# Optimization experiments

Hardware: AMD Instinct MI355X
Metric: run time of the kernel (lower is better)

The kernel has to match this reference:

```python
import jax, jax.numpy as jnp
import numpy as np

N_NODES = 100000
N_EDGES = 800000
N_GRAPHS = 256
IN_C = 96
HID = 96
OUT_C = 16


def setup_inputs() -> dict:
    key = jax.random.key(0)
    ks = jax.random.split(key, 10)
    x = jax.random.normal(ks[0], (N_NODES, IN_C), dtype=jnp.float32)
    edge_index = jax.random.randint(ks[1], (2, N_EDGES), 0, N_NODES, dtype=jnp.int64)
    batch = jnp.sort(jax.random.randint(ks[2], (N_NODES,), 0, N_GRAPHS, dtype=jnp.int64))
    def glorot(k, fan_in, fan_out):
        s = np.sqrt(6.0 / (fan_in + fan_out)).astype(np.float32)
        return jax.random.uniform(k, (fan_in, fan_out), minval=-s, maxval=s, dtype=jnp.float32)
    W1 = glorot(ks[3], IN_C, HID)
    W2 = glorot(ks[4], HID, HID)
    W3 = glorot(ks[5], HID, HID)
    Wlin = glorot(ks[6], HID, OUT_C)
    b1 = jnp.zeros((HID,), dtype=jnp.float32)
    b2 = jnp.zeros((HID,), dtype=jnp.float32)
    b3 = jnp.zeros((HID,), dtype=jnp.float32)
    return {"x": x, "edge_index": edge_index, "batch": batch,
            "W1": W1, "b1": b1, "W2": W2, "b2": b2, "W3": W3, "b3": b3, "Wlin": Wlin}


def _gcn_conv(x, W, b, src, dst):
    # PyG GCNConv(normalize=True): add self-loops, deg includes self-loop,
    # norm_ij = deg_i^{-1/2} * deg_j^{-1/2}; linear (no bias) then scatter-add; bias after.
    n = x.shape[0]
    deg = jnp.zeros((n,), dtype=x.dtype).at[dst].add(1.0) + 1.0  # +1 self-loop
    dinv = jax.lax.rsqrt(deg)
    h = x @ W                                   # [N, H]
    coef = dinv[src] * dinv[dst]                # [E]
    msg = h[src] * coef[:, None]                # [E, H] gather
    agg = jax.ops.segment_sum(msg, dst, num_segments=n)  # scatter-add
    agg = agg + h * (dinv * dinv)[:, None]      # self-loop contribution
    return agg + b


def reference(x, edge_index, batch, W1, b1, W2, b2, W3, b3, Wlin):
    src, dst = edge_index[0], edge_index[1]
    h = jax.nn.relu(_gcn_conv(x, W1, b1, src, dst))
    h = jax.nn.relu(_gcn_conv(h, W2, b2, src, dst))
    h = _gcn_conv(h, W3, b3, src, dst)
    # global mean pool over graphs
    sums = jax.ops.segment_sum(h, batch, num_segments=N_GRAPHS)
    counts = jax.ops.segment_sum(jnp.ones((h.shape[0],), dtype=h.dtype), batch, num_segments=N_GRAPHS)
    pooled = sums / jnp.maximum(counts, 1.0)[:, None]
    return pooled @ Wlin
```

## Files before the change

### kernel.cpp

```cpp
#include <hip/hip_runtime.h>

#define NN 100000
#define NE 800000
#define NG 256
#define CH 96
#define OC 16
#define NBLK 391
#define TM 128
#define GBLK 782

typedef __attribute__((ext_vector_type(8))) short bf16x8;
typedef __attribute__((ext_vector_type(4))) float f32x4;

__device__ __forceinline__ unsigned short f2bf(float x) {
    unsigned u = __float_as_uint(x);
    return (unsigned short)((u + 0x7fffu + ((u >> 16) & 1u)) >> 16);
}
__device__ __forceinline__ float bf2f(unsigned short h) {
    return __uint_as_float(((unsigned)h) << 16);
}
__device__ __forceinline__ void split8(const float4 a, const float4 b,
                                       bf16x8& hi, bf16x8& lo) {
    float v[8] = {a.x, a.y, a.z, a.w, b.x, b.y, b.z, b.w};
#pragma unroll
    for (int j = 0; j < 8; j++) {
        unsigned short h = f2bf(v[j]);
        hi[j] = (short)h;
        lo[j] = (short)f2bf(v[j] - bf2f(h));
    }
}
__device__ __forceinline__ float4 us4_to_f4(ushort4 u) {
    return make_float4(bf2f(u.x), bf2f(u.y), bf2f(u.z), bf2f(u.w));
}
__device__ __forceinline__ void unpack8(uint4 v, float* f) {
    f[0] = __uint_as_float(v.x << 16); f[1] = __uint_as_float(v.x & 0xffff0000u);
    f[2] = __uint_as_float(v.y << 16); f[3] = __uint_as_float(v.y & 0xffff0000u);
    f[4] = __uint_as_float(v.z << 16); f[5] = __uint_as_float(v.z & 0xffff0000u);
    f[6] = __uint_as_float(v.w << 16); f[7] = __uint_as_float(v.w & 0xffff0000u);
}

__global__ __launch_bounds__(256) void k_init(int* __restrict__ cntp,
                                              int* __restrict__ gtot,
                                              const float* __restrict__ W1,
                                              const float* __restrict__ W2,
                                              const float* __restrict__ W3,
                                              unsigned short* __restrict__ WH,
                                              unsigned short* __restrict__ WL) {
    int id = blockIdx.x * 256 + threadIdx.x;
    if (id < NN) {
        uint4 z = {0u, 0u, 0u, 0u};
        uint4* p = reinterpret_cast<uint4*>(&cntp[(size_t)id * 16]);
        p[0] = z; p[1] = z; p[2] = z; p[3] = z;
    }
    if (id == 0) *gtot = 0;
    if (id < 3 * CH * CH) {
        int w = id / (CH * CH);
        int r = id - w * (CH * CH);
        int k = r / CH;
        int n = r - k * CH;
        const float* Ws = (w == 0) ? W1 : (w == 1) ? W2 : W3;
        float v = Ws[k * CH + n];
        unsigned short h = f2bf(v);
        WH[w * CH * CH + n * CH + k] = h;
        WL[w * CH * CH + n * CH + k] = f2bf(v - bf2f(h));
    }
}

__global__ __launch_bounds__(256) void k_front(const float* __restrict__ X,
                                               const unsigned short* __restrict__ WH,
                                               const unsigned short* __restrict__ WL,
                                               unsigned short* __restrict__ H,
                                               const int* __restrict__ dst,
                                               int* __restrict__ cntp,
                                               int* __restrict__ slot) {
    __shared__ __align__(16) unsigned short WsH[CH * CH];
    __shared__ __align__(16) unsigned short WsL[CH * CH];

    const int tid = threadIdx.x;

    if (blockIdx.x >= GBLK) {
        int e = (blockIdx.x - GBLK) * 256 + tid;
        slot[e] = atomicAdd(&cntp[(size_t)dst[e] * 16], 1);
        return;
    }

    const int n0 = blockIdx.x * TM;
    {
        const uint4* sH = reinterpret_cast<const uint4*>(WH);
        const uint4* sL = reinterpret_cast<const uint4*>(WL);
        uint4* dH = reinterpret_cast<uint4*>(WsH);
        uint4* dL = reinterpret_cast<uint4*>(WsL);
        for (int i = tid; i < CH * CH / 8; i += 256) {
            dH[i] = sH[i];
            dL[i] = sL[i];
        }
    }
    __syncthreads();

    const int lane = tid & 63;
    const int wave = tid >> 6;
    const int lrow = lane & 15;
    const int quad = lane >> 4;

    const float4* X4 = reinterpret_cast<const float4*>(X);

    f32x4 acc[2][6];
#pragma unroll
    for (int rt = 0; rt < 2; rt++)
#pragma unroll
        for (int ct = 0; ct < 6; ct++) acc[rt][ct] = (f32x4){0.f, 0.f, 0.f, 0.f};

    int arow[2];
#pragma unroll
    for (int rt = 0; rt < 2; rt++)
        arow[rt] = min(n0 + (wave * 2 + rt) * 16 + lrow, NN - 1);

#pragma unroll
    for (int kc = 0; kc < 3; kc++) {
        bf16x8 ahi[2], alo[2];
#pragma unroll
        for (int rt = 0; rt < 2; rt++) {
            int fo = (arow[rt] * CH + kc * 32 + quad * 8) >> 2;
            split8(X4[fo], X4[fo + 1], ahi[rt], alo[rt]);
        }
#pragma unroll
        for (int ct = 0; ct < 6; ct++) {
            int bo = (ct * 16 + lrow) * CH + kc * 32 + quad * 8;
            bf16x8 bhi = *reinterpret_cast<const bf16x8*>(&WsH[bo]);
            bf16x8 blo = *reinterpret_cast<const bf16x8*>(&WsL[bo]);
#pragma unroll
            for (int rt = 0; rt < 2; rt++) {
                acc[rt][ct] = __builtin_amdgcn_mfma_f32_16x16x32_bf16(
                    alo[rt], bhi, acc[rt][ct], 0, 0, 0);
                acc[rt][ct] = __builtin_amdgcn_mfma_f32_16x16x32_bf16(
                    ahi[rt], blo, acc[rt][ct], 0, 0, 0);
                acc[rt][ct] = __builtin_amdgcn_mfma_f32_16x16x32_bf16(
                    ahi[rt], bhi, acc[rt][ct], 0, 0, 0);
            }
        }
    }

#pragma unroll
    for (int rt = 0; rt < 2; rt++) {
        int rbase = n0 + (wave * 2 + rt) * 16 + quad * 4;
#pragma unroll
        for (int ct = 0; ct < 6; ct++) {
            int col = ct * 16 + lrow;
#pragma unroll
            for (int r = 0; r < 4; r++) {
                int row = rbase + r;
                if (row < NN) H[(size_t)row * CH + col] = f2bf(acc[rt][ct][r]);
            }
        }
    }
}

__global__ __launch_bounds__(256) void k_offsets(const int* __restrict__ cntp,
                                                 int* __restrict__ cntc,
                                                 int* __restrict__ gtot,
                                                 int* __restrict__ off,
                                                 float* __restrict__ dinv,
                                                 const int* __restrict__ batch,
                                                 int* __restrict__ goff) {
    int i = blockIdx.x * 256 + threadIdx.x;
    int lane = threadIdx.x & 63;
    int c = (i < NN) ? cntp[(size_t)i * 16] : 0;

    int incl = c;
#pragma unroll
    for (int d = 1; d < 64; d <<= 1) {
        int t = __shfl_up(incl, d);
        if (lane >= d) incl += t;
    }
    int total = __shfl(incl, 63);
    int base = 0;
    if (lane == 63) base = atomicAdd(gtot, total);
    base = __shfl(base, 63);

    if (i >= NN) return;
    cntc[i] = c;
    off[i] = base + incl - c;
    dinv[i] = rsqrtf((float)c + 1.0f);
    int b = batch[i];
    int bp = (i > 0) ? batch[i - 1] : -1;
    for (int g = bp + 1; g <= b; g++) goff[g] = i;
    if (i == NN - 1)
        for (int g = b + 1; g <= NG; g++) goff[g] = NN;
}

__global__ __launch_bounds__(256) void k_build(const int* __restrict__ src,
                                               const int* __restrict__ dst,
                                               const int* __restrict__ off,
                                               const int* __restrict__ slot,
                                               const float* __restrict__ dinv,
                                               float2* __restrict__ packed) {
    int e = blockIdx.x * 256 + threadIdx.x;
    int s = src[e];
    int d = dst[e];
    packed[off[d] + slot[e]] = make_float2(__int_as_float(s), dinv[s] * dinv[d]);
}

__global__ __launch_bounds__(256) void k_gemm_bf16(const unsigned short* __restrict__ X,
                                                   const unsigned short* __restrict__ WH,
                                                   const unsigned short* __restrict__ WL,
                                                   unsigned short* __restrict__ H) {
    __shared__ __align__(16) unsigned short WsH[CH * CH];
    __shared__ __align__(16) unsigned short WsL[CH * CH];

    const int tid = threadIdx.x;
    const int n0 = blockIdx.x * TM;

    {
        const uint4* sH = reinterpret_cast<const uint4*>(WH);
        const uint4* sL = reinterpret_cast<const uint4*>(WL);
        uint4* dH = reinterpret_cast<uint4*>(WsH);
        uint4* dL = reinterpret_cast<uint4*>(WsL);
        for (int i = tid; i < CH * CH / 8; i += 256) {
            dH[i] = sH[i];
            dL[i] = sL[i];
        }
    }
    __syncthreads();

    const int lane = tid & 63;
    const int wave = tid >> 6;
    const int lrow = lane & 15;
    const int quad = lane >> 4;

    f32x4 acc[2][6];
#pragma unroll
    for (int rt = 0; rt < 2; rt++)
#pragma unroll
        for (int ct = 0; ct < 6; ct++) acc[rt][ct] = (f32x4){0.f, 0.f, 0.f, 0.f};

    int arow[2];
#pragma unroll
    for (int rt = 0; rt < 2; rt++)
        arow[rt] = min(n0 + (wave * 2 + rt) * 16 + lrow, NN - 1);

#pragma unroll
    for (int kc = 0; kc < 3; kc++) {
        bf16x8 ahi[2];
#pragma unroll
        for (int rt = 0; rt < 2; rt++)
            ahi[rt] = *reinterpret_cast<const bf16x8*>(
                &X[(size_t)arow[rt] * CH + kc * 32 + quad * 8]);
#pragma unroll
        for (int ct = 0; ct < 6; ct++) {
            int bo = (ct * 16 + lrow) * CH + kc * 32 + quad * 8;
            bf16x8 bhi = *reinterpret_cast<const bf16x8*>(&WsH[bo]);
            bf16x8 blo = *reinterpret_cast<const bf16x8*>(&WsL[bo]);
#pragma unroll
            for (int rt = 0; rt < 2; rt++) {
                acc[rt][ct] = __builtin_amdgcn_mfma_f32_16x16x32_bf16(
                    ahi[rt], blo, acc[rt][ct], 0, 0, 0);
                acc[rt][ct] = __builtin_amdgcn_mfma_f32_16x16x32_bf16(
                    ahi[rt], bhi, acc[rt][ct], 0, 0, 0);
            }
        }
    }

#pragma unroll
    for (int rt = 0; rt < 2; rt++) {
        int rbase = n0 + (wave * 2 + rt) * 16 + quad * 4;
#pragma unroll
        for (int ct = 0; ct < 6; ct++) {
            int col = ct * 16 + lrow;
#pragma unroll
            for (int r = 0; r < 4; r++) {
                int row = rbase + r;
                if (row < NN) H[(size_t)row * CH + col] = f2bf(acc[rt][ct][r]);
            }
        }
    }
}

template <bool RELU>
__global__ __launch_bounds__(256) void k_aggregate(const int* __restrict__ off,
                                                   const int* __restrict__ cnt,
                                                   const float2* __restrict__ packed,
                                                   const float* __restrict__ dinv,
                                                   const float* __restrict__ bias,
                                                   const unsigned short* __restrict__ H,
                                                   unsigned short* __restrict__ Bout) {
    int idx = blockIdx.x * 256 + threadIdx.x;
    if (idx >= NN * 12) return;
    int n = idx / 12;
    int c8 = idx - n * 12;
    int e0 = off[n];
    int e1 = e0 + cnt[n];

    const uint4* H8 = reinterpret_cast<const uint4*>(H);

    float a[8];
    {
        float hf[8];
        unpack8(H8[(size_t)n * 12 + c8], hf);
        float di = dinv[n];
        float d2 = di * di;
        const float4* bias4 = reinterpret_cast<const float4*>(bias);
        float4 b0 = bias4[c8 * 2], b1 = bias4[c8 * 2 + 1];
        float bf[8] = {b0.x, b0.y, b0.z, b0.w, b1.x, b1.y, b1.z, b1.w};
#pragma unroll
        for (int j = 0; j < 8; j++) a[j] = hf[j] * d2 + bf[j];
    }

    int e = e0;
    for (; e + 4 <= e1; e += 4) {
        float2 p0 = packed[e + 0];
        float2 p1 = packed[e + 1];
        float2 p2 = packed[e + 2];
        float2 p3 = packed[e + 3];
        uint4 v0 = H8[(size_t)__float_as_int(p0.x) * 12 + c8];
        uint4 v1 = H8[(size_t)__float_as_int(p1.x) * 12 + c8];
        uint4 v2 = H8[(size_t)__float_as_int(p2.x) * 12 + c8];
        uint4 v3 = H8[(size_t)__float_as_int(p3.x) * 12 + c8];
        float f0[8], f1[8], f2[8], f3[8];
        unpack8(v0, f0); unpack8(v1, f1); unpack8(v2, f2); unpack8(v3, f3);
#pragma unroll
        for (int j = 0; j < 8; j++)
            a[j] += f0[j] * p0.y + f1[j] * p1.y + f2[j] * p2.y + f3[j] * p3.y;
    }
    for (; e < e1; e++) {
        float2 pc = packed[e];
        uint4 v = H8[(size_t)__float_as_int(pc.x) * 12 + c8];
        float f[8];
        unpack8(v, f);
#pragma unroll
        for (int j = 0; j < 8; j++) a[j] += f[j] * pc.y;
    }
    if (RELU) {
#pragma unroll
        for (int j = 0; j < 8; j++) a[j] = fmaxf(a[j], 0.0f);
    }
    uint4 o;
    o.x = (unsigned)f2bf(a[0]) | ((unsigned)f2bf(a[1]) << 16);
    o.y = (unsigned)f2bf(a[2]) | ((unsigned)f2bf(a[3]) << 16);
    o.z = (unsigned)f2bf(a[4]) | ((unsigned)f2bf(a[5]) << 16);
    o.w = (unsigned)f2bf(a[6]) | ((unsigned)f2bf(a[7]) << 16);
    reinterpret_cast<uint4*>(Bout)[(size_t)n * 12 + c8] = o;
}

__global__ __launch_bounds__(384) void k_pool_linear(const int* __restrict__ goff,
                                                     const unsigned short* __restrict__ B,
                                                     const float* __restrict__ Wlin,
                                                     float* __restrict__ out) {
    __shared__ float4 sh[16][24];
    __shared__ float pooled[CH];
    int g = blockIdx.x;
    int t = threadIdx.x;
    int nl = t / 24;
    int c4 = t - nl * 24;
    int s = goff[g];
    int e = goff[g + 1];

    float4 acc = make_float4(0.f, 0.f, 0.f, 0.f);
    const ushort4* B4 = reinterpret_cast<const ushort4*>(B);
    for (int n = s + nl; n < e; n += 16) {
        float4 v = us4_to_f4(B4[(size_t)n * 24 + c4]);
        acc.x += v.x; acc.y += v.y; acc.z += v.z; acc.w += v.w;
    }
    sh[nl][c4] = acc;
    __syncthreads();

    if (t < 24) {
        float4 r = make_float4(0.f, 0.f, 0.f, 0.f);
#pragma unroll
        for (int j = 0; j < 16; j++) {
            float4 v = sh[j][t];
            r.x += v.x; r.y += v.y; r.z += v.z; r.w += v.w;
        }
        float inv = 1.0f / fmaxf((float)(e - s), 1.0f);
        pooled[t * 4 + 0] = r.x * inv;
        pooled[t * 4 + 1] = r.y * inv;
        pooled[t * 4 + 2] = r.z * inv;
        pooled[t * 4 + 3] = r.w * inv;
    }
    __syncthreads();

    if (t < OC) {
        float a = 0.0f;
#pragma unroll 8
        for (int k = 0; k < CH; k++) a += pooled[k] * Wlin[k * OC + t];
        out[g * OC + t] = a;
    }
}

extern "C" void kernel_launch(void* const* d_in, const int* in_sizes, int n_in,
                              void* d_out, int out_size, void* d_ws, size_t ws_size,
                              hipStream_t stream) {
    const float* x = (const float*)d_in[0];
    const int* ei = (const int*)d_in[1];
    const int* src = ei;
    const int* dst = ei + NE;
    const int* batch = (const int*)d_in[2];
    const float* W1 = (const float*)d_in[3];
    const float* b1 = (const float*)d_in[4];
    const float* W2 = (const float*)d_in[5];
    const float* b2 = (const float*)d_in[6];
    const float* W3 = (const float*)d_in[7];
    const float* b3 = (const float*)d_in[8];
    const float* Wlin = (const float*)d_in[9];
    float* out = (float*)d_out;

    char* ws = (char*)d_ws;
    unsigned short* Ha = (unsigned short*)ws;  ws += (size_t)NN * CH * 2;
    unsigned short* Hb = (unsigned short*)ws;  ws += (size_t)NN * CH * 2;
    unsigned short* Bb = (unsigned short*)ws;  ws += (size_t)NN * CH * 2;
    float2* packed = (float2*)ws;   ws += (size_t)NE * 8;
    unsigned short* WH = (unsigned short*)ws;  ws += 3 * CH * CH * 2;
    unsigned short* WL = (unsigned short*)ws;  ws += 3 * CH * CH * 2;
    float* dinv = (float*)ws;       ws += NN * 4;
    int* off = (int*)ws;            ws += NN * 4;
    int* goff = (int*)ws;           ws += 272 * 4;
    int* cntc = (int*)ws;           ws += (NN + 4) * 4;
    int* gtot = cntc + NN;
    int* cntp = (int*)Hb;
    int* slot = (int*)Bb;

    k_init<<<NBLK, 256, 0, stream>>>(cntp, gtot, W1, W2, W3, WH, WL);
    k_front<<<GBLK + NE / 256, 256, 0, stream>>>(x, WH, WL, Ha, dst, cntp, slot);
    k_offsets<<<NBLK, 256, 0, stream>>>(cntp, cntc, gtot, off, dinv, batch, goff);
    k_build<<<NE / 256, 256, 0, stream>>>(src, dst, off, slot, dinv, packed);

    const int ablk = (NN * 12 + 255) / 256;

    k_aggregate<true><<<ablk, 256, 0, stream>>>(off, cntc, packed, dinv, b1, Ha, Bb);
    k_gemm_bf16<<<GBLK, 256, 0, stream>>>(Bb, WH + CH * CH, WL + CH * CH, Hb);
    k_aggregate<true><<<ablk, 256, 0, stream>>>(off, cntc, packed, dinv, b2, Hb, Bb);
    k_gemm_bf16<<<GBLK, 256, 0, stream>>>(Bb, WH + 2 * CH * CH, WL + 2 * CH * CH, Ha);
    k_aggregate<false><<<ablk, 256, 0, stream>>>(off, cntc, packed, dinv, b3, Ha, Bb);

    k_pool_linear<<<NG, 384, 0, stream>>>(goff, Bb, Wlin, out);
}
```

Before: 299.2 us.

## Split degree histogram into per-lane sub-counters and separate from first GEMM

The per-node degree counter changes from one 64-byte-padded int to four sub-counters picked by edge index mod 4, which spreads atomic contention on a node. k_offsets sums the four counters and writes a sub-offset for each, and k_build uses those to place edges. The histogram also moves out of the fused front kernel into its own launch before the layer-1 GEMM. This removes the fusion that let atomics overlap the GEMM, adds a kernel launch, and changes the order of edges within each node's neighbour list.

```diff
diff --git a/kernel.cpp b/kernel.cpp
--- a/kernel.cpp
+++ b/kernel.cpp
@@ -8,6 +8,7 @@
 #define NBLK 391
 #define TM 128
 #define GBLK 782
+#define HBLK 3125
 
 typedef __attribute__((ext_vector_type(8))) short bf16x8;
 typedef __attribute__((ext_vector_type(4))) float f32x4;
@@ -39,7 +40,7 @@
     f[6] = __uint_as_float(v.w << 16); f[7] = __uint_as_float(v.w & 0xffff0000u);
 }
 
-__global__ __launch_bounds__(256) void k_init(int* __restrict__ cntp,
+__global__ __launch_bounds__(256) void k_init(int* __restrict__ cnt4,
                                               int* __restrict__ gtot,
                                               const float* __restrict__ W1,
                                               const float* __restrict__ W2,
@@ -49,8 +50,7 @@
     int id = blockIdx.x * 256 + threadIdx.x;
     if (id < NN) {
         uint4 z = {0u, 0u, 0u, 0u};
-        uint4* p = reinterpret_cast<uint4*>(&cntp[(size_t)id * 16]);
-        p[0] = z; p[1] = z; p[2] = z; p[3] = z;
+        *reinterpret_cast<uint4*>(&cnt4[(size_t)id * 4]) = z;
     }
     if (id == 0) *gtot = 0;
     if (id < 3 * CH * CH) {
@@ -66,24 +66,21 @@
     }
 }
 
-__global__ __launch_bounds__(256) void k_front(const float* __restrict__ X,
+__global__ __launch_bounds__(256) void k_hist(const int* __restrict__ dst,
+                                              int* __restrict__ cnt4,
+                                              int* __restrict__ slot) {
+    int e = blockIdx.x * 256 + threadIdx.x;
+    slot[e] = atomicAdd(&cnt4[(size_t)dst[e] * 4 + (e & 3)], 1);
+}
+
+__global__ __launch_bounds__(256) void k_gemm1(const float* __restrict__ X,
                                                const unsigned short* __restrict__ WH,
                                                const unsigned short* __restrict__ WL,
-                                               unsigned short* __restrict__ H,
-                                               const int* __restrict__ dst,
-                                               int* __restrict__ cntp,
-                                               int* __restrict__ slot) {
+                                               unsigned short* __restrict__ H) {
     __shared__ __align__(16) unsigned short WsH[CH * CH];
     __shared__ __align__(16) unsigned short WsL[CH * CH];
 
     const int tid = threadIdx.x;
-
-    if (blockIdx.x >= GBLK) {
-        int e = (blockIdx.x - GBLK) * 256 + tid;
-        slot[e] = atomicAdd(&cntp[(size_t)dst[e] * 16], 1);
-        return;
-    }
-
     const int n0 = blockIdx.x * TM;
     {
         const uint4* sH = reinterpret_cast<const uint4*>(WH);
@@ -155,7 +152,7 @@
     }
 }
 
-__global__ __launch_bounds__(256) void k_offsets(const int* __restrict__ cntp,
+__global__ __launch_bounds__(256) void k_offsets(int* __restrict__ cnt4,
                                                  int* __restrict__ cntc,
                                                  int* __restrict__ gtot,
                                                  int* __restrict__ off,
@@ -164,7 +161,9 @@
                                                  int* __restrict__ goff) {
     int i = blockIdx.x * 256 + threadIdx.x;
     int lane = threadIdx.x & 63;
-    int c = (i < NN) ? cntp[(size_t)i * 16] : 0;
+    int4 c4 = {0, 0, 0, 0};
+    if (i < NN) c4 = *reinterpret_cast<const int4*>(&cnt4[(size_t)i * 4]);
+    int c = c4.x + c4.y + c4.z + c4.w;
 
     int incl = c;
 #pragma unroll
@@ -178,8 +177,15 @@
     base = __shfl(base, 63);
 
     if (i >= NN) return;
+    int myoff = base + incl - c;
     cntc[i] = c;
-    off[i] = base + incl - c;
+    off[i] = myoff;
+    int4 w;
+    w.x = myoff;
+    w.y = myoff + c4.x;
+    w.z = myoff + c4.x + c4.y;
+    w.w = myoff + c4.x + c4.y + c4.z;
+    *reinterpret_cast<int4*>(&cnt4[(size_t)i * 4]) = w;
     dinv[i] = rsqrtf((float)c + 1.0f);
     int b = batch[i];
     int bp = (i > 0) ? batch[i - 1] : -1;
@@ -190,14 +196,15 @@
 
 __global__ __launch_bounds__(256) void k_build(const int* __restrict__ src,
                                                const int* __restrict__ dst,
-                                               const int* __restrict__ off,
+                                               const int* __restrict__ cnt4,
                                                const int* __restrict__ slot,
                                                const float* __restrict__ dinv,
                                                float2* __restrict__ packed) {
     int e = blockIdx.x * 256 + threadIdx.x;
     int s = src[e];
     int d = dst[e];
-    packed[off[d] + slot[e]] = make_float2(__int_as_float(s), dinv[s] * dinv[d]);
+    int p = cnt4[(size_t)d * 4 + (e & 3)] + slot[e];
+    packed[p] = make_float2(__int_as_float(s), dinv[s] * dinv[d]);
 }
 
 __global__ __launch_bounds__(256) void k_gemm_bf16(const unsigned short* __restrict__ X,
@@ -415,13 +422,14 @@
     int* goff = (int*)ws;           ws += 272 * 4;
     int* cntc = (int*)ws;           ws += (NN + 4) * 4;
     int* gtot = cntc + NN;
-    int* cntp = (int*)Hb;
+    int* cnt4 = (int*)Hb;
     int* slot = (int*)Bb;
 
-    k_init<<<NBLK, 256, 0, stream>>>(cntp, gtot, W1, W2, W3, WH, WL);
-    k_front<<<GBLK + NE / 256, 256, 0, stream>>>(x, WH, WL, Ha, dst, cntp, slot);
-    k_offsets<<<NBLK, 256, 0, stream>>>(cntp, cntc, gtot, off, dinv, batch, goff);
-    k_build<<<NE / 256, 256, 0, stream>>>(src, dst, off, slot, dinv, packed);
+    k_init<<<NBLK, 256, 0, stream>>>(cnt4, gtot, W1, W2, W3, WH, WL);
+    k_hist<<<HBLK, 256, 0, stream>>>(dst, cnt4, slot);
+    k_gemm1<<<GBLK, 256, 0, stream>>>(x, WH, WL, Ha);
+    k_offsets<<<NBLK, 256, 0, stream>>>(cnt4, cntc, gtot, off, dinv, batch, goff);
+    k_build<<<NE / 256, 256, 0, stream>>>(src, dst, cnt4, slot, dinv, packed);
 
     const int ablk = (NN * 12 + 255) / 256;
 
```

Result: slower. 313.4 us (+4.7%).

## Fold final linear into layer-3 weights to aggregate 16 channels instead of 96

Applied to the files above, without the earlier changes.

Because the last GCN layer, mean pooling and the output linear are all linear, W3·Wlin and b3·Wlin are precomputed in the init kernel. The third GEMM then produces only 16 columns, and the third aggregation gathers 16-wide rows instead of 96-wide ones. This cuts the gather traffic of the last aggregation and the pooling work by about six times. In exchange, the fused weight is rounded to bf16 hi/lo, which slightly changes numerical rounding.

```diff
diff --git a/kernel.cpp b/kernel.cpp
--- a/kernel.cpp
+++ b/kernel.cpp
@@ -29,9 +29,6 @@
         lo[j] = (short)f2bf(v[j] - bf2f(h));
     }
 }
-__device__ __forceinline__ float4 us4_to_f4(ushort4 u) {
-    return make_float4(bf2f(u.x), bf2f(u.y), bf2f(u.z), bf2f(u.w));
-}
 __device__ __forceinline__ void unpack8(uint4 v, float* f) {
     f[0] = __uint_as_float(v.x << 16); f[1] = __uint_as_float(v.x & 0xffff0000u);
     f[2] = __uint_as_float(v.y << 16); f[3] = __uint_as_float(v.y & 0xffff0000u);
@@ -44,8 +41,11 @@
                                               const float* __restrict__ W1,
                                               const float* __restrict__ W2,
                                               const float* __restrict__ W3,
+                                              const float* __restrict__ b3,
+                                              const float* __restrict__ Wlin,
                                               unsigned short* __restrict__ WH,
-                                              unsigned short* __restrict__ WL) {
+                                              unsigned short* __restrict__ WL,
+                                              float* __restrict__ b3p) {
     int id = blockIdx.x * 256 + threadIdx.x;
     if (id < NN) {
         uint4 z = {0u, 0u, 0u, 0u};
@@ -53,16 +53,32 @@
         p[0] = z; p[1] = z; p[2] = z; p[3] = z;
     }
     if (id == 0) *gtot = 0;
-    if (id < 3 * CH * CH) {
+    if (id < 2 * CH * CH) {
         int w = id / (CH * CH);
         int r = id - w * (CH * CH);
         int k = r / CH;
         int n = r - k * CH;
-        const float* Ws = (w == 0) ? W1 : (w == 1) ? W2 : W3;
+        const float* Ws = (w == 0) ? W1 : W2;
         float v = Ws[k * CH + n];
         unsigned short h = f2bf(v);
         WH[w * CH * CH + n * CH + k] = h;
         WL[w * CH * CH + n * CH + k] = f2bf(v - bf2f(h));
+    } else if (id < 2 * CH * CH + CH * OC) {
+        int r = id - 2 * CH * CH;
+        int k = r / OC;
+        int oc = r - k * OC;
+        float v = 0.0f;
+#pragma unroll 8
+        for (int m = 0; m < CH; m++) v += W3[k * CH + m] * Wlin[m * OC + oc];
+        unsigned short h = f2bf(v);
+        WH[2 * CH * CH + oc * CH + k] = h;
+        WL[2 * CH * CH + oc * CH + k] = f2bf(v - bf2f(h));
+    } else if (id < 2 * CH * CH + CH * OC + OC) {
+        int oc = id - 2 * CH * CH - CH * OC;
+        float v = 0.0f;
+#pragma unroll 8
+        for (int m = 0; m < CH; m++) v += b3[m] * Wlin[m * OC + oc];
+        b3p[oc] = v;
     }
 }
 
@@ -271,6 +287,70 @@
                 int row = rbase + r;
                 if (row < NN) H[(size_t)row * CH + col] = f2bf(acc[rt][ct][r]);
             }
+        }
+    }
+}
+
+__global__ __launch_bounds__(256) void k_gemm3(const unsigned short* __restrict__ X,
+                                               const unsigned short* __restrict__ WH,
+                                               const unsigned short* __restrict__ WL,
+                                               unsigned short* __restrict__ H3) {
+    __shared__ __align__(16) unsigned short WsH[OC * CH];
+    __shared__ __align__(16) unsigned short WsL[OC * CH];
+
+    const int tid = threadIdx.x;
+    const int n0 = blockIdx.x * TM;
+
+    {
+        const uint4* sH = reinterpret_cast<const uint4*>(WH);
+        const uint4* sL = reinterpret_cast<const uint4*>(WL);
+        uint4* dH = reinterpret_cast<uint4*>(WsH);
+        uint4* dL = reinterpret_cast<uint4*>(WsL);
+        for (int i = tid; i < OC * CH / 8; i += 256) {
+            dH[i] = sH[i];
+            dL[i] = sL[i];
+        }
+    }
+    __syncthreads();
+
+    const int lane = tid & 63;
+    const int wave = tid >> 6;
+    const int lrow = lane & 15;
+    const int quad = lane >> 4;
+
+    f32x4 acc[2];
+#pragma unroll
+    for (int rt = 0; rt < 2; rt++) acc[rt] = (f32x4){0.f, 0.f, 0.f, 0.f};
+
+    int arow[2];
+#pragma unroll
+    for (int rt = 0; rt < 2; rt++)
+        arow[rt] = min(n0 + (wave * 2 + rt) * 16 + lrow, NN - 1);
+
+#pragma unroll
+    for (int kc = 0; kc < 3; kc++) {
+        bf16x8 ahi[2];
+#pragma unroll
+        for (int rt = 0; rt < 2; rt++)
+            ahi[rt] = *reinterpret_cast<const bf16x8*>(
+                &X[(size_t)arow[rt] * CH + kc * 32 + quad * 8]);
+        int bo = lrow * CH + kc * 32 + quad * 8;
+        bf16x8 bhi = *reinterpret_cast<const bf16x8*>(&WsH[bo]);
+        bf16x8 blo = *reinterpret_cast<const bf16x8*>(&WsL[bo]);
+#pragma unroll
+        for (int rt = 0; rt < 2; rt++) {
+            acc[rt] = __builtin_amdgcn_mfma_f32_16x16x32_bf16(ahi[rt], blo, acc[rt], 0, 0, 0);
+            acc[rt] = __builtin_amdgcn_mfma_f32_16x16x32_bf16(ahi[rt], bhi, acc[rt], 0, 0, 0);
+        }
+    }
+
+#pragma unroll
+    for (int rt = 0; rt < 2; rt++) {
+        int rbase = n0 + (wave * 2 + rt) * 16 + quad * 4;
+#pragma unroll
+        for (int r = 0; r < 4; r++) {
+            int row = rbase + r;
+            if (row < NN) H3[(size_t)row * OC + lrow] = f2bf(acc[rt][r]);
         }
     }
 }
@@ -341,48 +421,83 @@
     reinterpret_cast<uint4*>(Bout)[(size_t)n * 12 + c8] = o;
 }
 
-__global__ __launch_bounds__(384) void k_pool_linear(const int* __restrict__ goff,
-                                                     const unsigned short* __restrict__ B,
-                                                     const float* __restrict__ Wlin,
-                                                     float* __restrict__ out) {
-    __shared__ float4 sh[16][24];
-    __shared__ float pooled[CH];
+__global__ __launch_bounds__(256) void k_agg16(const int* __restrict__ off,
+                                               const int* __restrict__ cnt,
+                                               const float2* __restrict__ packed,
+                                               const float* __restrict__ dinv,
+                                               const unsigned short* __restrict__ H3,
+                                               float* __restrict__ B3) {
+    int idx = blockIdx.x * 256 + threadIdx.x;
+    if (idx >= NN * 2) return;
+    int n = idx >> 1;
+    int c8 = idx & 1;
+    int e0 = off[n];
+    int e1 = e0 + cnt[n];
+
+    const uint4* H8 = reinterpret_cast<const uint4*>(H3);
+
+    float a[8];
+    {
+        float hf[8];
+        unpack8(H8[(size_t)n * 2 + c8], hf);
+        float di = dinv[n];
+        float d2 = di * di;
+#pragma unroll
+        for (int j = 0; j < 8; j++) a[j] = hf[j] * d2;
+    }
+
+    int e = e0;
+    for (; e + 4 <= e1; e += 4) {
+        float2 p0 = packed[e + 0];
+        float2 p1 = packed[e + 1];
+        float2 p2 = packed[e + 2];
+        float2 p3 = packed[e + 3];
+        uint4 v0 = H8[(size_t)__float_as_int(p0.x) * 2 + c8];
+        uint4 v1 = H8[(size_t)__float_as_int(p1.x) * 2 + c8];
+        uint4 v2 = H8[(size_t)__float_as_int(p2.x) * 2 + c8];
+        uint4 v3 = H8[(size_t)__float_as_int(p3.x) * 2 + c8];
+        float f0[8], f1[8], f2[8], f3[8];
+        unpack8(v0, f0); unpack8(v1, f1); unpack8(v2, f2); unpack8(v3, f3);
+#pragma unroll
+        for (int j = 0; j < 8; j++)
+            a[j] += f0[j] * p0.y + f1[j] * p1.y + f2[j] * p2.y + f3[j] * p3.y;
+    }
+    for (; e < e1; e++) {
+        float2 pc = packed[e];
+        uint4 v = H8[(size_t)__float_as_int(pc.x) * 2 + c8];
+        float f[8];
+        unpack8(v, f);
+#pragma unroll
+        for (int j = 0; j < 8; j++) a[j] += f[j] * pc.y;
+    }
+
+    float4* B4 = reinterpret_cast<float4*>(B3);
+    B4[(size_t)n * 4 + c8 * 2 + 0] = make_float4(a[0], a[1], a[2], a[3]);
+    B4[(size_t)n * 4 + c8 * 2 + 1] = make_float4(a[4], a[5], a[6], a[7]);
+}
+
+__global__ __launch_bounds__(256) void k_pool16(const int* __restrict__ goff,
+                                                const float* __restrict__ B3,
+                                                const float* __restrict__ b3p,
+                                                float* __restrict__ out) {
+    __shared__ float sh[16][16];
     int g = blockIdx.x;
     int t = threadIdx.x;
-    int nl = t / 24;
-    int c4 = t - nl * 24;
+    int ch = t & 15;
+    int nl = t >> 4;
     int s = goff[g];
     int e = goff[g + 1];
 
-    float4 acc = make_float4(0.f, 0.f, 0.f, 0.f);
-    const ushort4* B4 = reinterpret_cast<const ushort4*>(B);
-    for (int n = s + nl; n < e; n += 16) {
-        float4 v = us4_to_f4(B4[(size_t)n * 24 + c4]);
-        acc.x += v.x; acc.y += v.y; acc.z += v.z; acc.w += v.w;
-    }
-    sh[nl][c4] = acc;
+    float acc = 0.0f;
+    for (int n = s + nl; n < e; n += 16) acc += B3[(size_t)n * OC + ch];
+    sh[nl][ch] = acc;
     __syncthreads();
 
-    if (t < 24) {
-        float4 r = make_float4(0.f, 0.f, 0.f, 0.f);
-#pragma unroll
-        for (int j = 0; j < 16; j++) {
-            float4 v = sh[j][t];
-            r.x += v.x; r.y += v.y; r.z += v.z; r.w += v.w;
-        }
-        float inv = 1.0f / fmaxf((float)(e - s), 1.0f);
-        pooled[t * 4 + 0] = r.x * inv;
-        pooled[t * 4 + 1] = r.y * inv;
-        pooled[t * 4 + 2] = r.z * inv;
-        pooled[t * 4 + 3] = r.w * inv;
-    }
-    __syncthreads();
-
     if (t < OC) {
-        float a = 0.0f;
-#pragma unroll 8
-        for (int k = 0; k < CH; k++) a += pooled[k] * Wlin[k * OC + t];
-        out[g * OC + t] = a;
+        float r = 0.0f;
+#pragma unroll
+        for (int j = 0; j < 16; j++) r += sh[j][t];
+        out[g * OC + t] = r / fmaxf((float)(e - s), 1.0f) + b3p[t];
     }
 }
 
@@ -415,10 +530,13 @@
     int* goff = (int*)ws;           ws += 272 * 4;
     int* cntc = (int*)ws;           ws += (NN + 4) * 4;
     int* gtot = cntc + NN;
+    float* b3p = (float*)ws;        ws += 64;
     int* cntp = (int*)Hb;
     int* slot = (int*)Bb;
-
-    k_init<<<NBLK, 256, 0, stream>>>(cntp, gtot, W1, W2, W3, WH, WL);
+    unsigned short* H3 = Ha;
+    float* B3 = (float*)Hb;
+
+    k_init<<<NBLK, 256, 0, stream>>>(cntp, gtot, W1, W2, W3, b3, Wlin, WH, WL, b3p);
     k_front<<<GBLK + NE / 256, 256, 0, stream>>>(x, WH, WL, Ha, dst, cntp, slot);
     k_offsets<<<NBLK, 256, 0, stream>>>(cntp, cntc, gtot, off, dinv, batch, goff);
     k_build<<<NE / 256, 256, 0, stream>>>(src, dst, off, slot, dinv, packed);
@@ -428,8 +546,7 @@
     k_aggregate<true><<<ablk, 256, 0, stream>>>(off, cntc, packed, dinv, b1, Ha, Bb);
     k_gemm_bf16<<<GBLK, 256, 0, stream>>>(Bb, WH + CH * CH, WL + CH * CH, Hb);
     k_aggregate<true><<<ablk, 256, 0, stream>>>(off, cntc, packed, dinv, b2, Hb, Bb);
-    k_gemm_bf16<<<GBLK, 256, 0, stream>>>(Bb, WH + 2 * CH * CH, WL + 2 * CH * CH, Ha);
-    k_aggregate<false><<<ablk, 256, 0, stream>>>(off, cntc, packed, dinv, b3, Ha, Bb);
-
-    k_pool_linear<<<NG, 384, 0, stream>>>(goff, Bb, Wlin, out);
-}
+    k_gemm3<<<GBLK, 256, 0, stream>>>(Bb, WH + 2 * CH * CH, WL + 2 * CH * CH, H3);
+    k_agg16<<<(NN * 2 + 255) / 256, 256, 0, stream>>>(off, cntc, packed, dinv, H3, B3);
+    k_pool16<<<NG, 256, 0, stream>>>(goff, B3, b3p, out);
+}
```

Measured after the change: 273.3 us. 8.7% less time.
